# Performance work log

Measured on AMD Instinct MI355X. Metric: run time of the kernel, lower is better.

Reference implementation:

```python
import jax, jax.numpy as jnp
import numpy as np

B, L, D = 4, 2048, 2048
H, KVH, HD = 16, 4, 128          # num_heads, num_kv_heads, head_dim = D // H
M = 16                           # mem_tokens
BASE = 10000.0
EPS = 1.1920929e-07              # torch F.rms_norm default eps = fp32 machine eps


def _rms_norm(x):
    # normalize over last dim, no learned weight (matches F.rms_norm(x, (hd,)))
    return x * jax.lax.rsqrt(jnp.mean(x * x, axis=-1, keepdims=True) + EPS)


def _apply_rotary(x, cos, sin):
    # x: [B, h, T, HD]; cos/sin: [1, 1, T, HD//2]
    half = x.shape[-1] // 2
    x1, x2 = x[..., :half], x[..., half:]
    return jnp.concatenate([x1 * cos + x2 * sin, -x1 * sin + x2 * cos], axis=-1)


def setup_inputs() -> dict:
    key = jax.random.key(0)
    k0, k1, k2, k3, k4 = jax.random.split(key, 5)
    kv_dim = KVH * HD
    s = 0.02
    return {
        "x": jax.random.normal(k0, (B, L, D), dtype=jnp.float32),
        "Wq": jax.random.normal(k1, (D, D), dtype=jnp.float32) * s,
        "Wk": jax.random.normal(k2, (kv_dim, D), dtype=jnp.float32) * s,
        "Wv": jax.random.normal(k3, (kv_dim, D), dtype=jnp.float32) * s,
        "Wproj": jax.random.normal(k4, (D, D), dtype=jnp.float32) * s,
        "q_gain": jnp.full((H,), 1.0, dtype=jnp.float32),
    }


def reference(x, Wq, Wk, Wv, Wproj, q_gain):
    Bx, Lx, Dx = x.shape
    # QKV projections (Linear: x @ W.T), split into heads -> [B, h, L, HD]
    q = (x @ Wq.T).reshape(Bx, Lx, H, HD).transpose(0, 2, 1, 3)
    k = (x @ Wk.T).reshape(Bx, Lx, KVH, HD).transpose(0, 2, 1, 3)
    v = (x @ Wv.T).reshape(Bx, Lx, KVH, HD).transpose(0, 2, 1, 3)
    # QK RMSNorm
    q = _rms_norm(q)
    k = _rms_norm(k)
    # RoPE on the non-memory tokens only
    T = Lx - M
    inv_freq = 1.0 / BASE ** (jnp.arange(0, HD, 2, dtype=jnp.float32) / HD)
    freqs = jnp.outer(jnp.arange(T, dtype=jnp.float32), inv_freq)  # [T, HD//2]
    cos = jnp.cos(freqs)[None, None]
    sin = jnp.sin(freqs)[None, None]
    q = jnp.concatenate([q[:, :, :M], _apply_rotary(q[:, :, M:], cos, sin)], axis=2)
    k = jnp.concatenate([k[:, :, :M], _apply_rotary(k[:, :, M:], cos, sin)], axis=2)
    # per-head gain on q
    q = q * q_gain[None, :, None, None]
    # GQA attention: group q heads by kv head (matches repeat_interleave ordering)
    rep = H // KVH
    qg = q.reshape(Bx, KVH, rep, Lx, HD)
    scale = 1.0 / np.sqrt(HD).astype(np.float32)
    scores = jnp.einsum('bgrqd,bgkd->bgrqk', qg, k) * scale  # [B, KVH, rep, L, L]
    causal = jnp.tril(jnp.ones((Lx, Lx), dtype=bool))
    scores = jnp.where(causal, scores, -jnp.inf)
    p = jax.nn.softmax(scores, axis=-1)
    y = jnp.einsum('bgrqk,bgkd->bgrqd', p, v)                # [B, KVH, rep, L, HD]
    y = y.reshape(Bx, H, Lx, HD).transpose(0, 2, 1, 3).reshape(Bx, Lx, Dx)
    return y @ Wproj.T
```

## Files before the change

kernel.cpp:

```cpp
#include <hip/hip_runtime.h>
#include <stdint.h>

typedef unsigned short u16;
typedef short s8v __attribute__((ext_vector_type(8)));
typedef float f4v __attribute__((ext_vector_type(4)));
typedef float f16v __attribute__((ext_vector_type(16)));

typedef __attribute__((address_space(1))) char gchar;
typedef __attribute__((address_space(3))) char lchar;

static __device__ __forceinline__ u16 f2bf(float f) {
  uint32_t x = __float_as_uint(f);
  x += 0x7fffu + ((x >> 16) & 1u);
  return (u16)(x >> 16);
}
static __device__ __forceinline__ float bf2f(u16 u) {
  return __uint_as_float(((uint32_t)u) << 16);
}
static __device__ __forceinline__ void gload_lds16(const void* g, void* l) {
  __builtin_amdgcn_global_load_lds((gchar*)(uintptr_t)g,
                                   (lchar*)(uint32_t)(uintptr_t)l, 16, 0, 0);
}

__global__ __launch_bounds__(256) void cvt_bf16(const float4* __restrict__ src,
                                                uint2* __restrict__ dst, int n4) {
  int i = blockIdx.x * 256 + threadIdx.x;
  int st = gridDim.x * 256;
  for (; i < n4; i += st) {
    float4 v = src[i];
    uint2 o;
    o.x = (uint32_t)f2bf(v.x) | ((uint32_t)f2bf(v.y) << 16);
    o.y = (uint32_t)f2bf(v.z) | ((uint32_t)f2bf(v.w) << 16);
    dst[i] = o;
  }
}

__global__ __launch_bounds__(256) void cvt_bf16_w(const float4* __restrict__ s0,
                                                  const float4* __restrict__ s1,
                                                  const float4* __restrict__ s2,
                                                  const float4* __restrict__ s3,
                                                  uint2* __restrict__ dst) {
  int i = blockIdx.x * 256 + threadIdx.x;
  int st = gridDim.x * 256;
  for (; i < 2621440; i += st) {
    const float4* s;
    int off;
    if (i < 1048576)      { s = s0; off = i; }
    else if (i < 1310720) { s = s1; off = i - 1048576; }
    else if (i < 1572864) { s = s2; off = i - 1310720; }
    else                  { s = s3; off = i - 1572864; }
    float4 v = s[off];
    uint2 o;
    o.x = (uint32_t)f2bf(v.x) | ((uint32_t)f2bf(v.y) << 16);
    o.y = (uint32_t)f2bf(v.z) | ((uint32_t)f2bf(v.w) << 16);
    dst[i] = o;
  }
}

__global__ __launch_bounds__(256) void rope_table(float* __restrict__ tc,
                                                  float* __restrict__ ts) {
  int i = blockIdx.x * 256 + threadIdx.x;
  if (i >= 2032 * 64) return;
  int t = i >> 6, f = i & 63;
  float invf = 1.0f / powf(10000.0f, (float)f * (1.0f / 64.0f));
  float ang = (float)t * invf;
  float s, c;
  sincosf(ang, &s, &c);
  tc[i] = c;
  ts[i] = s;
}

template <int MODE>
__global__ __launch_bounds__(512, 2) void gemm_nt(
    const u16* __restrict__ A, const u16* __restrict__ W0,
    const u16* __restrict__ W1, const u16* __restrict__ W2,
    u16* __restrict__ O0, u16* __restrict__ O1, u16* __restrict__ O2,
    float* __restrict__ OF) {
  __shared__ u16 lA[2][256 * 64];
  __shared__ u16 lB[2][256 * 64];
  const int tid = threadIdx.x;
  const int lane = tid & 63, wid = tid >> 6;
  const int wr = wid >> 2, wc = wid & 3;
  const int l15 = lane & 15, l4 = lane >> 4;

  const int nwg = gridDim.x;
  const int bid = blockIdx.x;
  const int swz = (bid & 7) * (nwg >> 3) + (bid >> 3);
  const int bn = swz >> 5, bm = swz & 31;
  const int m0 = bm * 256;

  const u16* Wt;
  int n0r;
  if constexpr (MODE == 0) {
    if (bn < 8)       { Wt = W0; n0r = bn * 256; }
    else if (bn < 10) { Wt = W1; n0r = (bn - 8) * 256; }
    else              { Wt = W2; n0r = (bn - 10) * 256; }
  } else {
    Wt = W0; n0r = bn * 256;
  }

  auto stage = [&](int kt, int bsel) {
    const int kb = kt * 64;
#pragma unroll
    for (int c = 0; c < 4; ++c) {
      int cidx = tid + c * 512;
      int r = cidx >> 3, s = cidx & 7;
      gload_lds16(A + (size_t)(m0 + r) * 2048 + kb + ((s ^ (r & 7)) * 8),
                  &lA[bsel][cidx * 8]);
    }
#pragma unroll
    for (int c = 0; c < 4; ++c) {
      int cidx = tid + c * 512;
      int r = cidx >> 3, s = cidx & 7;
      gload_lds16(Wt + (size_t)(n0r + r) * 2048 + kb + ((s ^ (r & 7)) * 8),
                  &lB[bsel][cidx * 8]);
    }
  };
  auto swzoff = [&](int fr, int s) {
    return fr * 64 + (((s) ^ (fr & 7)) << 3);
  };

  const f4v Z4 = {0.f, 0.f, 0.f, 0.f};
  f4v acc[8][4];
#pragma unroll
  for (int i = 0; i < 8; i++)
#pragma unroll
    for (int j = 0; j < 4; j++) acc[i][j] = Z4;

  stage(0, 0);

  const int NT = 32;
  for (int t = 0; t < NT; ++t) {
    const int cur = t & 1;
    asm volatile("s_waitcnt lgkmcnt(0)" ::: "memory");
    __builtin_amdgcn_sched_barrier(0);
    asm volatile("s_barrier" ::: "memory");
    if (t + 1 < NT) {
      stage(t + 1, cur ^ 1);
      asm volatile("s_waitcnt vmcnt(8)" ::: "memory");
    } else {
      asm volatile("s_waitcnt vmcnt(0)" ::: "memory");
    }
    asm volatile("s_barrier" ::: "memory");

    const u16* pa = &lA[cur][0];
    const u16* pb = &lB[cur][0];
#pragma unroll
    for (int ks = 0; ks < 2; ++ks) {
      s8v afrg[8], bfrg[4];
#pragma unroll
      for (int i = 0; i < 8; ++i)
        afrg[i] = *(const s8v*)&pa[swzoff(wr * 128 + i * 16 + l15, ks * 4 + l4)];
#pragma unroll
      for (int j = 0; j < 4; ++j)
        bfrg[j] = *(const s8v*)&pb[swzoff(wc * 64 + j * 16 + l15, ks * 4 + l4)];
      __builtin_amdgcn_s_setprio(1);
#pragma unroll
      for (int i = 0; i < 8; ++i)
#pragma unroll
        for (int j = 0; j < 4; ++j)
          acc[i][j] = __builtin_amdgcn_mfma_f32_16x16x32_bf16(afrg[i], bfrg[j], acc[i][j], 0, 0, 0);
      __builtin_amdgcn_s_setprio(0);
    }
  }

  const int ncol0 = bn * 256 + wc * 64;
  if constexpr (MODE == 0) {
    const int colg = ncol0;
    u16* Ob; int hh, HX;
    if (colg < 2048)      { Ob = O0; hh = colg >> 7;          HX = 16; }
    else if (colg < 2560) { Ob = O1; hh = (colg - 2048) >> 7; HX = 4; }
    else                  { Ob = O2; hh = (colg - 2560) >> 7; HX = 4; }
    const int d0 = colg & 127;
#pragma unroll
    for (int i = 0; i < 8; i++)
#pragma unroll
      for (int r = 0; r < 4; r++) {
        int m = m0 + wr * 128 + i * 16 + l4 * 4 + r;
        int b = m >> 11, l = m & 2047;
        size_t base = ((size_t)(b * HX + hh) * 2048 + l) * 128 + d0;
#pragma unroll
        for (int j = 0; j < 4; j++)
          Ob[base + j * 16 + l15] = f2bf(acc[i][j][r]);
      }
  } else {
#pragma unroll
    for (int i = 0; i < 8; i++)
#pragma unroll
      for (int r = 0; r < 4; r++) {
        int m = m0 + wr * 128 + i * 16 + l4 * 4 + r;
#pragma unroll
        for (int j = 0; j < 4; j++)
          OF[(size_t)m * 2048 + ncol0 + j * 16 + l15] = acc[i][j][r];
      }
  }
}

__global__ __launch_bounds__(256) void norm_rope(u16* __restrict__ buf,
                                                 const float* __restrict__ gain,
                                                 const float* __restrict__ tc,
                                                 const float* __restrict__ ts) {
  const int lane = threadIdx.x & 63;
  const int gw = blockIdx.x * 4 + (threadIdx.x >> 6);
  const int nw = gridDim.x * 4;
  for (int row = gw; row < 163840; row += nw) {
    int l = row & 2047;
    u16* p = buf + (size_t)row * 128;
    float x1 = bf2f(p[lane]);
    float x2 = bf2f(p[lane + 64]);
    float ss = x1 * x1 + x2 * x2;
#pragma unroll
    for (int off = 32; off > 0; off >>= 1) ss += __shfl_xor(ss, off, 64);
    float r = rsqrtf(ss * (1.0f / 128.0f) + 1.1920929e-07f);
    x1 *= r; x2 *= r;
    if (l >= 16) {
      int t = l - 16;
      float c = tc[t * 64 + lane], s = ts[t * 64 + lane];
      float o1 = x1 * c + x2 * s;
      float o2 = -x1 * s + x2 * c;
      x1 = o1; x2 = o2;
    }
    if (row < 131072) {
      float g = gain[(row >> 11) & 15] *
                (0.08838834764831845f * 1.4426950408889634f);
      x1 *= g; x2 *= g;
    }
    p[lane] = f2bf(x1);
    p[lane + 64] = f2bf(x2);
  }
}

__global__ __launch_bounds__(256) void transpose_v(const u16* __restrict__ v,
                                                   u16* __restrict__ vt) {
  __shared__ u16 t[64][64];
  const int l0 = blockIdx.x * 64, d0 = blockIdx.y * 64, bg = blockIdx.z;
  const int tid = threadIdx.x;
#pragma unroll
  for (int it = 0; it < 2; ++it) {
    int lin = it * 256 + tid;
    int r = lin >> 3, cb = lin & 7;
    s8v val = *(const s8v*)&v[((bg * 2048 + l0 + r) * 128) + d0 + cb * 8];
    *(s8v*)&t[r][(cb ^ (r & 7)) * 8] = val;
  }
  __syncthreads();
#pragma unroll
  for (int it = 0; it < 2; ++it) {
    int lin = it * 256 + tid;
    int r2 = lin >> 3, c2 = (lin & 7) * 8;
    s8v o;
#pragma unroll
    for (int j = 0; j < 8; ++j) {
      int rr = c2 + j, cc = r2;
      o[j] = (short)t[rr][(cc & 7) + 8 * ((cc >> 3) ^ (rr & 7))];
    }
    *(s8v*)&vt[((bg * 128 + d0 + r2) * 2048) + l0 + c2] = o;
  }
}

__global__ __launch_bounds__(256, 2) void attn(const u16* __restrict__ q,
                                               const u16* __restrict__ k,
                                               const u16* __restrict__ vt,
                                               u16* __restrict__ y) {
  __shared__ u16 lK[2][64 * 128];
  __shared__ u16 lVT[2][128 * 64];
  const int tid = threadIdx.x;
  const int lane = tid & 63, wid = tid >> 6;
  const int l31 = lane & 31, hi = lane >> 5;

  const int db = (int)blockIdx.y * 32 + (int)blockIdx.x;
  const int half = db >> 8, rem = db & 255;
  const int bg = (rem & 7) + 8 * half;
  const int pairi = rem >> 3;
  const int b = bg >> 2, g = bg & 3;
  const int h = g * 4 + wid;

  const u16* qh = q + (size_t)(b * 16 + h) * 2048 * 128;
  const u16* kb0 = k + (size_t)(b * 4 + g) * 2048 * 128;
  const u16* vtb0 = vt + (size_t)(b * 4 + g) * 128 * 2048;

  auto stage = [&](int t, int bufsel) {
    const int kv0 = t * 64;
#pragma unroll
    for (int it = 0; it < 4; ++it) {
      int lin = it * 256 + tid;
      int kj = lin >> 4, s = lin & 15;
      gload_lds16(kb0 + (size_t)(kv0 + kj) * 128 + ((s ^ (kj & 7)) * 8),
                  &lK[bufsel][lin * 8]);
    }
#pragma unroll
    for (int it = 0; it < 4; ++it) {
      int lin = it * 256 + tid;
      int d = lin >> 3, s = lin & 7;
      gload_lds16(vtb0 + (size_t)d * 2048 + kv0 + ((s ^ (d & 7)) * 8),
                  &lVT[bufsel][lin * 8]);
    }
  };

  for (int ph = 0; ph < 2; ++ph) {
    const int qt = ph ? (63 - pairi) : pairi;
    const int q0 = qt * 32;
    const int nt = (q0 >> 6) + 1;
    const int qabs = q0 + l31;

    s8v qf[8];
#pragma unroll
    for (int ks = 0; ks < 8; ++ks)
      qf[ks] = *(const s8v*)&qh[(q0 + l31) * 128 + ks * 16 + hi * 8];

    f16v yacc[4];
#pragma unroll
    for (int j = 0; j < 4; ++j)
#pragma unroll
      for (int r = 0; r < 16; ++r) yacc[j][r] = 0.f;
    float mrow = -1e30f, lrow = 0.f;

    stage(0, 0);
    __syncthreads();

    for (int t = 0; t < nt; ++t) {
      const int cur = t & 1;
      if (t + 1 < nt) stage(t + 1, cur ^ 1);
      const int kv0 = t * 64;

      f16v s0a, s1a;
#pragma unroll
      for (int r = 0; r < 16; ++r) { s0a[r] = 0.f; s1a[r] = 0.f; }
      __builtin_amdgcn_s_setprio(1);
#pragma unroll
      for (int ks = 0; ks < 8; ++ks) {
        const int slot = (2 * ks + hi) ^ (l31 & 7);
        s8v kf0 = *(const s8v*)&lK[cur][(l31)*128 + slot * 8];
        s8v kf1 = *(const s8v*)&lK[cur][(32 + l31) * 128 + slot * 8];
        s0a = __builtin_amdgcn_mfma_f32_32x32x16_bf16(kf0, qf[ks], s0a, 0, 0, 0);
        s1a = __builtin_amdgcn_mfma_f32_32x32x16_bf16(kf1, qf[ks], s1a, 0, 0, 0);
      }
      __builtin_amdgcn_s_setprio(0);

      const bool last = (t == nt - 1);
      float p0[16], p1[16];
      float pmax = -1e30f;
#pragma unroll
      for (int r = 0; r < 16; ++r) {
        const int kvloc = (r & 3) + 8 * (r >> 2) + 4 * hi;
        float v0 = s0a[r];
        float v1 = s1a[r];
        if (last) {
          if (kv0 + kvloc > qabs) v0 = -1e30f;
          if (kv0 + 32 + kvloc > qabs) v1 = -1e30f;
        }
        p0[r] = v0; p1[r] = v1;
        pmax = fmaxf(pmax, fmaxf(v0, v1));
      }
      pmax = fmaxf(pmax, __shfl_xor(pmax, 32, 64));

      if (!__all(pmax - mrow <= 11.541560327111707f)) {
        float mnew = fmaxf(mrow, pmax);
        float corr = __builtin_amdgcn_exp2f(mrow - mnew);
#pragma unroll
        for (int r = 0; r < 16; ++r) {
          const int qloc = (r & 3) + 8 * (r >> 2) + 4 * hi;
          float cb = __shfl(corr, qloc, 64);
          yacc[0][r] *= cb; yacc[1][r] *= cb; yacc[2][r] *= cb; yacc[3][r] *= cb;
        }
        lrow *= corr;
        mrow = mnew;
      }

      float ps = 0.f;
#pragma unroll
      for (int r = 0; r < 16; ++r) {
        float e0 = __builtin_amdgcn_exp2f(p0[r] - mrow);
        float e1 = __builtin_amdgcn_exp2f(p1[r] - mrow);
        p0[r] = e0; p1[r] = e1;
        ps += e0 + e1;
      }
      ps += __shfl_xor(ps, 32, 64);
      lrow += ps;

      __builtin_amdgcn_s_setprio(1);
#pragma unroll
      for (int ks = 0; ks < 4; ++ks) {
        const float* pc = (ks < 2) ? p0 : p1;
        const int rb = 8 * (ks & 1);
        uint32_t A0, A1, B0, B1;
        asm("v_cvt_pk_bf16_f32 %0, %1, %2" : "=v"(A0) : "v"(pc[rb + 0]), "v"(pc[rb + 1]));
        asm("v_cvt_pk_bf16_f32 %0, %1, %2" : "=v"(A1) : "v"(pc[rb + 2]), "v"(pc[rb + 3]));
        asm("v_cvt_pk_bf16_f32 %0, %1, %2" : "=v"(B0) : "v"(pc[rb + 4]), "v"(pc[rb + 5]));
        asm("v_cvt_pk_bf16_f32 %0, %1, %2" : "=v"(B1) : "v"(pc[rb + 6]), "v"(pc[rb + 7]));
        uint32_t t0 = hi ? A0 : B0;
        uint32_t t1 = hi ? A1 : B1;
        uint32_t r0 = (uint32_t)__shfl_xor((int)t0, 32, 64);
        uint32_t r1 = (uint32_t)__shfl_xor((int)t1, 32, 64);
        union { uint32_t u[4]; s8v v; } uu;
        uu.u[0] = hi ? r0 : A0;
        uu.u[1] = hi ? r1 : A1;
        uu.u[2] = hi ? B0 : r0;
        uu.u[3] = hi ? B1 : r1;
#pragma unroll
        for (int jd = 0; jd < 4; ++jd) {
          const int rowd = 32 * jd + l31;
          const int slot = (2 * ks + hi) ^ (l31 & 7);
          s8v vf = *(const s8v*)&lVT[cur][rowd * 64 + slot * 8];
          yacc[jd] = __builtin_amdgcn_mfma_f32_32x32x16_bf16(uu.v, vf, yacc[jd], 0, 0, 0);
        }
      }
      __builtin_amdgcn_s_setprio(0);
      __syncthreads();
    }

    float inv = 1.0f / lrow;
#pragma unroll
    for (int r = 0; r < 16; ++r) {
      const int qloc = (r & 3) + 8 * (r >> 2) + 4 * hi;
      float ib = __shfl(inv, qloc, 64);
      const int qrow = q0 + qloc;
      size_t base = ((size_t)(b * 2048 + qrow)) * 2048 + h * 128 + l31;
#pragma unroll
      for (int jd = 0; jd < 4; ++jd)
        y[base + 32 * jd] = f2bf(yacc[jd][r] * ib);
    }
  }
}

extern "C" void kernel_launch(void* const* d_in, const int* in_sizes, int n_in,
                              void* d_out, int out_size, void* d_ws, size_t ws_size,
                              hipStream_t stream) {
  const float* x  = (const float*)d_in[0];
  const float* Wq = (const float*)d_in[1];
  const float* Wk = (const float*)d_in[2];
  const float* Wv = (const float*)d_in[3];
  const float* Wp = (const float*)d_in[4];
  const float* qg = (const float*)d_in[5];
  float* out = (float*)d_out;

  char* ws = (char*)d_ws;
  size_t off = 0;
  auto alloc = [&](size_t bytes) {
    void* p = ws + off;
    off += (bytes + 255) & ~(size_t)255;
    return p;
  };
  u16* x_bf  = (u16*)alloc((size_t)8192 * 2048 * 2);
  u16* wq_bf = (u16*)alloc((size_t)2048 * 2048 * 2);
  u16* wk_bf = (u16*)alloc((size_t)512 * 2048 * 2);
  u16* wv_bf = (u16*)alloc((size_t)512 * 2048 * 2);
  u16* wp_bf = (u16*)alloc((size_t)2048 * 2048 * 2);
  u16* q_bf  = (u16*)alloc((size_t)4 * 16 * 2048 * 128 * 2);
  u16* k_bf  = (u16*)alloc((size_t)4 * 4 * 2048 * 128 * 2);
  u16* v_bf  = (u16*)alloc((size_t)4 * 4 * 2048 * 128 * 2);
  float* tab = (float*)alloc((size_t)2032 * 64 * 2 * 4);
  u16* y_bf  = x_bf;
  u16* vt_bf = wq_bf;

  cvt_bf16<<<2048, 256, 0, stream>>>((const float4*)x, (uint2*)x_bf, 8192 * 2048 / 4);
  cvt_bf16_w<<<1024, 256, 0, stream>>>((const float4*)Wq, (const float4*)Wk,
                                       (const float4*)Wv, (const float4*)Wp,
                                       (uint2*)wq_bf);
  rope_table<<<(2032 * 64 + 255) / 256, 256, 0, stream>>>(tab, tab + 2032 * 64);

  gemm_nt<0><<<dim3(384), 512, 0, stream>>>(x_bf, wq_bf, wk_bf, wv_bf,
                                            q_bf, k_bf, v_bf, nullptr);
  norm_rope<<<2048, 256, 0, stream>>>(q_bf, qg, tab, tab + 2032 * 64);
  transpose_v<<<dim3(32, 2, 16), 256, 0, stream>>>(v_bf, vt_bf);
  attn<<<dim3(32, 16), 256, 0, stream>>>(q_bf, k_bf, vt_bf, y_bf);
  gemm_nt<1><<<dim3(256), 512, 0, stream>>>(y_bf, wp_bf, nullptr, nullptr,
                                            nullptr, nullptr, nullptr, out);
}
```

Before: 349.7 us.

## Split QKV GEMM into Q and KV launches with half-K triple-stage prefetch

The fused 384-block QKV GEMM becomes two launches of 256 blocks each. The Q projection uses 256-wide N tiles, and the K/V projection uses 128-wide N tiles so the grid fills the device evenly instead of running 1.5 waves. The LDS tiles are split into two 32-wide K halves with a new swizzle, and loads are now issued two tiles ahead, refilling each half right after its fragments are read. This overlaps global loads with MFMA more deeply, at the cost of an extra kernel launch and more barriers per iteration.

```diff
diff --git a/kernel.cpp b/kernel.cpp
--- a/kernel.cpp
+++ b/kernel.cpp
@@ -70,93 +70,86 @@
   ts[i] = s;
 }
 
-template <int MODE>
+template <int BN, int OUT>
 __global__ __launch_bounds__(512, 2) void gemm_nt(
-    const u16* __restrict__ A, const u16* __restrict__ W0,
-    const u16* __restrict__ W1, const u16* __restrict__ W2,
-    u16* __restrict__ O0, u16* __restrict__ O1, u16* __restrict__ O2,
-    float* __restrict__ OF) {
-  __shared__ u16 lA[2][256 * 64];
-  __shared__ u16 lB[2][256 * 64];
+    const u16* __restrict__ A, const u16* __restrict__ Wt,
+    u16* __restrict__ Oa, u16* __restrict__ Ob2, float* __restrict__ OF) {
+  constexpr int MI = (BN == 256) ? 8 : 4;
+  constexpr int BLOADS = (BN == 256) ? 2 : 1;
+  __shared__ u16 lA[2][2][256 * 32];
+  __shared__ u16 lB[2][2][BN * 32];
   const int tid = threadIdx.x;
   const int lane = tid & 63, wid = tid >> 6;
-  const int wr = wid >> 2, wc = wid & 3;
+  const int wr = (BN == 256) ? (wid >> 2) : (wid >> 1);
+  const int wc = (BN == 256) ? (wid & 3) : (wid & 1);
   const int l15 = lane & 15, l4 = lane >> 4;
 
-  const int nwg = gridDim.x;
   const int bid = blockIdx.x;
-  const int swz = (bid & 7) * (nwg >> 3) + (bid >> 3);
+  const int swz = (bid & 7) * 32 + (bid >> 3);
   const int bn = swz >> 5, bm = swz & 31;
   const int m0 = bm * 256;
-
-  const u16* Wt;
-  int n0r;
-  if constexpr (MODE == 0) {
-    if (bn < 8)       { Wt = W0; n0r = bn * 256; }
-    else if (bn < 10) { Wt = W1; n0r = (bn - 8) * 256; }
-    else              { Wt = W2; n0r = (bn - 10) * 256; }
-  } else {
-    Wt = W0; n0r = bn * 256;
-  }
-
-  auto stage = [&](int kt, int bsel) {
-    const int kb = kt * 64;
-#pragma unroll
-    for (int c = 0; c < 4; ++c) {
+  const int n0r = bn * BN;
+
+  auto stage_part = [&](int kt, int bs, int ks) {
+    const int kb = kt * 64 + ks * 32;
+#pragma unroll
+    for (int c = 0; c < 2; ++c) {
       int cidx = tid + c * 512;
-      int r = cidx >> 3, s = cidx & 7;
-      gload_lds16(A + (size_t)(m0 + r) * 2048 + kb + ((s ^ (r & 7)) * 8),
-                  &lA[bsel][cidx * 8]);
-    }
-#pragma unroll
-    for (int c = 0; c < 4; ++c) {
+      int r = cidx >> 2, q = cidx & 3;
+      int cc = q ^ ((r >> 2) & 3);
+      gload_lds16(A + (size_t)(m0 + r) * 2048 + kb + cc * 8,
+                  &lA[bs][ks][cidx * 8]);
+    }
+#pragma unroll
+    for (int c = 0; c < BLOADS; ++c) {
       int cidx = tid + c * 512;
-      int r = cidx >> 3, s = cidx & 7;
-      gload_lds16(Wt + (size_t)(n0r + r) * 2048 + kb + ((s ^ (r & 7)) * 8),
-                  &lB[bsel][cidx * 8]);
+      int r = cidx >> 2, q = cidx & 3;
+      int cc = q ^ ((r >> 2) & 3);
+      gload_lds16(Wt + (size_t)(n0r + r) * 2048 + kb + cc * 8,
+                  &lB[bs][ks][cidx * 8]);
     }
   };
-  auto swzoff = [&](int fr, int s) {
-    return fr * 64 + (((s) ^ (fr & 7)) << 3);
+  auto roff = [&](int fr, int c) {
+    return (fr * 4 + (c ^ ((fr >> 2) & 3))) * 8;
   };
 
   const f4v Z4 = {0.f, 0.f, 0.f, 0.f};
-  f4v acc[8][4];
-#pragma unroll
-  for (int i = 0; i < 8; i++)
+  f4v acc[MI][4];
+#pragma unroll
+  for (int i = 0; i < MI; i++)
 #pragma unroll
     for (int j = 0; j < 4; j++) acc[i][j] = Z4;
 
-  stage(0, 0);
+  stage_part(0, 0, 0); stage_part(0, 0, 1);
+  stage_part(1, 1, 0); stage_part(1, 1, 1);
 
   const int NT = 32;
   for (int t = 0; t < NT; ++t) {
-    const int cur = t & 1;
-    asm volatile("s_waitcnt lgkmcnt(0)" ::: "memory");
-    __builtin_amdgcn_sched_barrier(0);
-    asm volatile("s_barrier" ::: "memory");
+    const int bs = t & 1;
     if (t + 1 < NT) {
-      stage(t + 1, cur ^ 1);
-      asm volatile("s_waitcnt vmcnt(8)" ::: "memory");
+      if constexpr (BN == 256) asm volatile("s_waitcnt vmcnt(8)" ::: "memory");
+      else                     asm volatile("s_waitcnt vmcnt(6)" ::: "memory");
     } else {
       asm volatile("s_waitcnt vmcnt(0)" ::: "memory");
     }
     asm volatile("s_barrier" ::: "memory");
-
-    const u16* pa = &lA[cur][0];
-    const u16* pb = &lB[cur][0];
+    const bool pf = (t + 2 < NT);
 #pragma unroll
     for (int ks = 0; ks < 2; ++ks) {
-      s8v afrg[8], bfrg[4];
-#pragma unroll
-      for (int i = 0; i < 8; ++i)
-        afrg[i] = *(const s8v*)&pa[swzoff(wr * 128 + i * 16 + l15, ks * 4 + l4)];
+      s8v afrg[MI], bfrg[4];
+#pragma unroll
+      for (int i = 0; i < MI; ++i)
+        afrg[i] = *(const s8v*)&lA[bs][ks][roff(wr * (MI * 16) + i * 16 + l15, l4)];
 #pragma unroll
       for (int j = 0; j < 4; ++j)
-        bfrg[j] = *(const s8v*)&pb[swzoff(wc * 64 + j * 16 + l15, ks * 4 + l4)];
+        bfrg[j] = *(const s8v*)&lB[bs][ks][roff(wc * 64 + j * 16 + l15, l4)];
+      asm volatile("s_waitcnt lgkmcnt(0)" ::: "memory");
+      __builtin_amdgcn_sched_barrier(0);
+      asm volatile("s_barrier" ::: "memory");
+      if (pf) stage_part(t + 2, bs, ks);
       __builtin_amdgcn_s_setprio(1);
 #pragma unroll
-      for (int i = 0; i < 8; ++i)
+      for (int i = 0; i < MI; ++i)
 #pragma unroll
         for (int j = 0; j < 4; ++j)
           acc[i][j] = __builtin_amdgcn_mfma_f32_16x16x32_bf16(afrg[i], bfrg[j], acc[i][j], 0, 0, 0);
@@ -164,34 +157,43 @@
     }
   }
 
-  const int ncol0 = bn * 256 + wc * 64;
-  if constexpr (MODE == 0) {
-    const int colg = ncol0;
-    u16* Ob; int hh, HX;
-    if (colg < 2048)      { Ob = O0; hh = colg >> 7;          HX = 16; }
-    else if (colg < 2560) { Ob = O1; hh = (colg - 2048) >> 7; HX = 4; }
-    else                  { Ob = O2; hh = (colg - 2560) >> 7; HX = 4; }
-    const int d0 = colg & 127;
-#pragma unroll
-    for (int i = 0; i < 8; i++)
+  const int colg = bn * BN + wc * 64;
+  if constexpr (OUT == 0) {
+    const int hh = colg >> 7, d0 = colg & 127;
+#pragma unroll
+    for (int i = 0; i < MI; i++)
 #pragma unroll
       for (int r = 0; r < 4; r++) {
-        int m = m0 + wr * 128 + i * 16 + l4 * 4 + r;
+        int m = m0 + wr * (MI * 16) + i * 16 + l4 * 4 + r;
         int b = m >> 11, l = m & 2047;
-        size_t base = ((size_t)(b * HX + hh) * 2048 + l) * 128 + d0;
+        size_t base = ((size_t)(b * 16 + hh) * 2048 + l) * 128 + d0;
+#pragma unroll
+        for (int j = 0; j < 4; j++)
+          Oa[base + j * 16 + l15] = f2bf(acc[i][j][r]);
+      }
+  } else if constexpr (OUT == 1) {
+    u16* Ob = (colg < 512) ? Oa : Ob2;
+    const int hh = (colg & 511) >> 7, d0 = colg & 127;
+#pragma unroll
+    for (int i = 0; i < MI; i++)
+#pragma unroll
+      for (int r = 0; r < 4; r++) {
+        int m = m0 + wr * (MI * 16) + i * 16 + l4 * 4 + r;
+        int b = m >> 11, l = m & 2047;
+        size_t base = ((size_t)(b * 4 + hh) * 2048 + l) * 128 + d0;
 #pragma unroll
         for (int j = 0; j < 4; j++)
           Ob[base + j * 16 + l15] = f2bf(acc[i][j][r]);
       }
   } else {
 #pragma unroll
-    for (int i = 0; i < 8; i++)
+    for (int i = 0; i < MI; i++)
 #pragma unroll
       for (int r = 0; r < 4; r++) {
-        int m = m0 + wr * 128 + i * 16 + l4 * 4 + r;
+        int m = m0 + wr * (MI * 16) + i * 16 + l4 * 4 + r;
 #pragma unroll
         for (int j = 0; j < 4; j++)
-          OF[(size_t)m * 2048 + ncol0 + j * 16 + l15] = acc[i][j][r];
+          OF[(size_t)m * 2048 + colg + j * 16 + l15] = acc[i][j][r];
       }
   }
 }
@@ -458,11 +460,10 @@
                                        (uint2*)wq_bf);
   rope_table<<<(2032 * 64 + 255) / 256, 256, 0, stream>>>(tab, tab + 2032 * 64);
 
-  gemm_nt<0><<<dim3(384), 512, 0, stream>>>(x_bf, wq_bf, wk_bf, wv_bf,
-                                            q_bf, k_bf, v_bf, nullptr);
+  gemm_nt<256, 0><<<dim3(256), 512, 0, stream>>>(x_bf, wq_bf, q_bf, nullptr, nullptr);
+  gemm_nt<128, 1><<<dim3(256), 512, 0, stream>>>(x_bf, wk_bf, k_bf, v_bf, nullptr);
   norm_rope<<<2048, 256, 0, stream>>>(q_bf, qg, tab, tab + 2032 * 64);
   transpose_v<<<dim3(32, 2, 16), 256, 0, stream>>>(v_bf, vt_bf);
   attn<<<dim3(32, 16), 256, 0, stream>>>(q_bf, k_bf, vt_bf, y_bf);
-  gemm_nt<1><<<dim3(256), 512, 0, stream>>>(y_bf, wp_bf, nullptr, nullptr,
-                                            nullptr, nullptr, nullptr, out);
-}
+  gemm_nt<256, 2><<<dim3(256), 512, 0, stream>>>(y_bf, wp_bf, nullptr, nullptr, out);
+}
```

After: 357.1 us. 1.02x slower.
